# Optimization experiments

Hardware: AMD Instinct MI355X
Metric: run time of the kernel (lower is better)

The kernel has to match this reference:

```python
import jax, jax.numpy as jnp
import numpy as np

B, S, E, H, Dh = 4, 2048, 2048, 16, 128
EPS = 1e-6

def rms_norm(x, scale):
    # RMSNorm over last dim (the module calls it LayerNorm but uses mean of squares)
    x = x.astype(jnp.float32)
    mean2 = jnp.mean(jnp.square(x), axis=-1, keepdims=True)
    return (x * jax.lax.rsqrt(mean2 + EPS)) * scale

def setup_inputs() -> dict:
    key = jax.random.key(0)
    ks = jax.random.split(key, 8)
    sd = 1.0 / np.sqrt(E)
    Wq = jax.random.normal(ks[0], (E, H, Dh), jnp.float32) * sd / np.sqrt(Dh)  # query_init divides by sqrt(head_dim)
    Wk = jax.random.normal(ks[1], (E, H, Dh), jnp.float32) * sd
    Wv = jax.random.normal(ks[2], (E, H, Dh), jnp.float32) * sd
    Wo = jax.random.normal(ks[3], (H, Dh, E), jnp.float32) * (1.0 / np.sqrt(H * Dh))
    return {
        "inputs_q": jax.random.normal(ks[4], (B, S, E), jnp.float32),
        "inputs_kv": jax.random.normal(ks[5], (B, S, E), jnp.float32),
        "Wq": Wq, "Wk": Wk, "Wv": Wv,
        "q_ln_scale": jnp.ones((Dh,), jnp.float32),
        "k_ln_scale": jnp.ones((Dh,), jnp.float32),
        "Wo": Wo,
    }

def reference(inputs_q, inputs_kv, Wq, Wk, Wv, q_ln_scale, k_ln_scale, Wo):
    # QKV projections: [B,S,E] x [E,H,Dh] -> [B,S,H,Dh]
    q = jnp.einsum('bqe,ehd->bqhd', inputs_q, Wq)
    k = jnp.einsum('bke,ehd->bkhd', inputs_kv, Wk)
    v = jnp.einsum('bke,ehd->bkhd', inputs_kv, Wv)
    # QK RMS-norm before attention (the non-standard fusion-defeating step)
    q = rms_norm(q, q_ln_scale)
    k = rms_norm(k, k_ln_scale)
    # attention logits and softmax (no mask/bias, deterministic)
    logits = jnp.einsum('bqhd,bkhd->bhqk', q, k)
    probs = jax.nn.softmax(logits, axis=-1)
    # weighted values and output projection
    ctx = jnp.einsum('bhqk,bkhd->bqhd', probs, v)
    out = jnp.einsum('bqhd,hde->bqe', ctx, Wo)
    return out
```

## Files before the change

### kernel.cpp

```cpp
#include <hip/hip_runtime.h>
#include <hip/hip_bf16.h>

typedef unsigned short u16;
typedef unsigned int u32;
typedef _Float16 f16;
typedef __attribute__((ext_vector_type(8))) short bf16x8;
typedef __attribute__((ext_vector_type(8))) _Float16 f16x8;
typedef __attribute__((ext_vector_type(4))) float f32x4;
typedef __attribute__((ext_vector_type(4))) u16 u16x4;

__device__ __forceinline__ float bf2f(u16 u){ return __uint_as_float(((u32)u) << 16); }
__device__ __forceinline__ u16 f2bf(float f){
  u32 u = __float_as_uint(f);
  u += 0x7fffu + ((u >> 16) & 1u);
  return (u16)(u >> 16);
}
__device__ __forceinline__ void gll16(const u16* g, u16* l){
  __builtin_amdgcn_global_load_lds((const __attribute__((address_space(1))) u32*)g,
                                   (__attribute__((address_space(3))) u32*)l, 16, 0, 0);
}

#define MFMA16(a,b,c) __builtin_amdgcn_mfma_f32_16x16x32_bf16((a),(b),(c),0,0,0)
#define MFMAH(a,b,c)  __builtin_amdgcn_mfma_f32_16x16x32_f16((a),(b),(c),0,0,0)

__global__ __launch_bounds__(256) void cvt_f16_2(const float* __restrict__ in0, const float* __restrict__ in1,
                                                 u16* __restrict__ out0, u16* __restrict__ out1){
  const int half = blockIdx.x >> 13;
  const float* in = half ? in1 : in0;
  u16* out = half ? out1 : out0;
  const size_t i = ((size_t)(blockIdx.x & 8191)*256 + threadIdx.x)*8;
  f16 h[8];
  #pragma unroll
  for (int j=0;j<8;j++) h[j] = (f16)in[i+j];
  *(f16x8*)(out+i) = *(f16x8*)h;
}

__global__ __launch_bounds__(256) void transpose_w4(const float* __restrict__ w0, const float* __restrict__ w1,
                                                    const float* __restrict__ w2, const float* __restrict__ w3,
                                                    u16* __restrict__ o0, u16* __restrict__ o1,
                                                    u16* __restrict__ o2, u16* __restrict__ o3){
  const int z = blockIdx.z;
  const float* in = (z==0) ? w0 : (z==1) ? w1 : (z==2) ? w2 : w3;
  u16* oh = (z==0) ? o0 : (z==1) ? o1 : (z==2) ? o2 : o3;
  __shared__ float tile[64*68];
  const int t = threadIdx.x;
  const int r0 = blockIdx.y*64, c0 = blockIdx.x*64;
  #pragma unroll
  for (int p=0;p<2;p++){
    const int row = p*32 + (t>>3), cg = (t&7)*8;
    const float* s = in + (size_t)(r0+row)*2048 + c0 + cg;
    #pragma unroll
    for (int j=0;j<8;j++) tile[row*68 + cg + j] = s[j];
  }
  __syncthreads();
  #pragma unroll
  for (int p=0;p<2;p++){
    const int orow = p*32 + (t>>3), cg = (t&7)*8;
    f16 h[8];
    #pragma unroll
    for (int j=0;j<8;j++) h[j] = (f16)(tile[(cg+j)*68 + orow] * 256.f);
    *(f16x8*)(oh + (size_t)(c0+orow)*2048 + r0 + cg) = *(f16x8*)h;
  }
}

template<int EPI>
__global__ __launch_bounds__(512, 1) void gemm8(const u16* __restrict__ A,
                                                const u16* __restrict__ Bt,
                                                const float* __restrict__ scale,
                                                u16* __restrict__ C,
                                                float* __restrict__ Cf){
  constexpr int K = 2048, NT = 32;
  __shared__ __align__(16) u16 AL[2][2][8192];
  __shared__ __align__(16) u16 BL[2][2][8192];
  __shared__ float red[2][4][128];

  const int t = threadIdx.x;
  const int lane = t & 63, w = t >> 6;
  const int wm = w >> 2, wn = w & 3;
  const int l15 = lane & 15, l4 = lane >> 4;

  const int bid = blockIdx.x;
  const int xcd = bid & 7, q = bid >> 3;
  const int m0 = (((xcd >> 1) << 3) + (q >> 2)) * 256;
  const int n0 = (((xcd & 1) << 2) + (q & 3)) * 256;

  const int srow = t >> 2;
  const int skg = (t & 3) ^ ((srow ^ (srow >> 2)) & 3);
  const u16* gA = A  + (size_t)(m0 + srow) * K + skg * 8;
  const u16* gB = Bt + (size_t)(n0 + srow) * K + skg * 8;
  const int d0 = (w * 64) * 8;
  const int d1 = (512 + w * 64) * 8;

  const int sz = (l15 ^ (l15 >> 2)) & 3;
  const int kgp = ((l4 ^ sz) & 3) * 8;
  const int aoff = (wm * 128 + l15) * 32 + kgp;
  const int boff = (wn * 64 + l15) * 32 + kgp;

  f32x4 acc[8][4] = {};

#define STG_A(tile, kh, db) { const u16* s_ = gA + (size_t)(tile)*64 + (kh)*32; \
    gll16(s_, &AL[db][kh][0] + d0); gll16(s_ + (size_t)128*K, &AL[db][kh][0] + d1); }
#define STG_B(tile, kh, db) { const u16* s_ = gB + (size_t)(tile)*64 + (kh)*32; \
    gll16(s_, &BL[db][kh][0] + d0); gll16(s_ + (size_t)128*K, &BL[db][kh][0] + d1); }

  STG_A(0,0,0); STG_B(0,0,0);
  STG_A(0,1,0); STG_B(0,1,0);
  STG_A(1,0,1); STG_B(1,0,1);
  asm volatile("s_waitcnt vmcnt(4)" ::: "memory");
  __builtin_amdgcn_s_barrier();

  for (int g = 0; g < NT; ++g){
    const int db = g & 1, db1 = db ^ 1;
    const int t1 = (g+1 < NT) ? g+1 : NT-1;
    const int t2 = (g+2 < NT) ? g+2 : NT-1;
    f16x8 a[4], b[4];

    #pragma unroll
    for (int nf=0; nf<4; nf++) b[nf] = *(const f16x8*)&BL[db][0][boff + nf*512];
    #pragma unroll
    for (int mf=0; mf<4; mf++) a[mf] = *(const f16x8*)&AL[db][0][aoff + mf*512];
    STG_A(t1, 1, db1);
    __builtin_amdgcn_s_barrier();
    asm volatile("s_waitcnt lgkmcnt(0)" ::: "memory");
    __builtin_amdgcn_sched_barrier(0);
    __builtin_amdgcn_s_setprio(1);
    #pragma unroll
    for (int mf=0; mf<4; mf++)
      #pragma unroll
      for (int nf=0; nf<4; nf++)
        acc[mf][nf] = MFMAH(a[mf], b[nf], acc[mf][nf]);
    __builtin_amdgcn_s_setprio(0);
    __builtin_amdgcn_s_barrier();

    #pragma unroll
    for (int mf=0; mf<4; mf++) a[mf] = *(const f16x8*)&AL[db][0][aoff + (mf+4)*512];
    STG_B(t1, 1, db1);
    __builtin_amdgcn_s_barrier();
    asm volatile("s_waitcnt lgkmcnt(0)" ::: "memory");
    __builtin_amdgcn_sched_barrier(0);
    __builtin_amdgcn_s_setprio(1);
    #pragma unroll
    for (int mf=0; mf<4; mf++)
      #pragma unroll
      for (int nf=0; nf<4; nf++)
        acc[mf+4][nf] = MFMAH(a[mf], b[nf], acc[mf+4][nf]);
    __builtin_amdgcn_s_setprio(0);
    __builtin_amdgcn_s_barrier();

    #pragma unroll
    for (int nf=0; nf<4; nf++) b[nf] = *(const f16x8*)&BL[db][1][boff + nf*512];
    #pragma unroll
    for (int mf=0; mf<4; mf++) a[mf] = *(const f16x8*)&AL[db][1][aoff + mf*512];
    STG_A(t2, 0, db);
    __builtin_amdgcn_s_barrier();
    asm volatile("s_waitcnt lgkmcnt(0)" ::: "memory");
    __builtin_amdgcn_sched_barrier(0);
    __builtin_amdgcn_s_setprio(1);
    #pragma unroll
    for (int mf=0; mf<4; mf++)
      #pragma unroll
      for (int nf=0; nf<4; nf++)
        acc[mf][nf] = MFMAH(a[mf], b[nf], acc[mf][nf]);
    __builtin_amdgcn_s_setprio(0);
    __builtin_amdgcn_s_barrier();

    #pragma unroll
    for (int mf=0; mf<4; mf++) a[mf] = *(const f16x8*)&AL[db][1][aoff + (mf+4)*512];
    STG_B(t2, 0, db);
    __builtin_amdgcn_s_barrier();
    asm volatile("s_waitcnt lgkmcnt(0)" ::: "memory");
    __builtin_amdgcn_sched_barrier(0);
    __builtin_amdgcn_s_setprio(1);
    #pragma unroll
    for (int mf=0; mf<4; mf++)
      #pragma unroll
      for (int nf=0; nf<4; nf++)
        acc[mf+4][nf] = MFMAH(a[mf], b[nf], acc[mf+4][nf]);
    __builtin_amdgcn_s_setprio(0);
    asm volatile("s_waitcnt vmcnt(4)" ::: "memory");
    __builtin_amdgcn_s_barrier();
  }

  asm volatile("s_waitcnt vmcnt(0)" ::: "memory");
  __builtin_amdgcn_s_barrier();

  const float us = 1.f/256.f;
  if (EPI == 0){
    #pragma unroll
    for (int mf=0; mf<8; mf++)
      #pragma unroll
      for (int nf=0; nf<4; nf++)
        #pragma unroll
        for (int r=0;r<4;r++) acc[mf][nf][r] *= us;
    #pragma unroll
    for (int mf=0; mf<8; mf++){
      #pragma unroll
      for (int r=0;r<4;r++){
        float p = acc[mf][0][r]*acc[mf][0][r] + acc[mf][1][r]*acc[mf][1][r]
                + acc[mf][2][r]*acc[mf][2][r] + acc[mf][3][r]*acc[mf][3][r];
        #pragma unroll
        for (int d=1; d<16; d<<=1) p += __shfl_xor(p, d, 64);
        if (l15 == 0) red[wm][wn][mf*16 + l4*4 + r] = p;
      }
    }
    __syncthreads();
    float sc[4];
    #pragma unroll
    for (int nf=0; nf<4; nf++) sc[nf] = scale[(wn*64 + nf*16 + l15) & 127];
    #pragma unroll
    for (int mf=0; mf<8; mf++){
      #pragma unroll
      for (int r=0;r<4;r++){
        const int rl = mf*16 + l4*4 + r;
        const float inv = rsqrtf((red[wm][wn & 2][rl] + red[wm][(wn & 2) | 1][rl])*(1.f/128.f) + 1e-6f);
        const size_t grow = (size_t)(m0 + wm*128 + rl);
        #pragma unroll
        for (int nf=0; nf<4; nf++){
          f16 hv = (f16)(acc[mf][nf][r]*inv*sc[nf]);
          C[grow*2048 + (n0 + wn*64 + nf*16 + l15)] = *reinterpret_cast<u16*>(&hv);
        }
      }
    }
  } else if (EPI == 1){
    #pragma unroll
    for (int mf=0; mf<8; mf++){
      const int m = m0 + wm*128 + mf*16 + l4*4;
      const int bb = m >> 11, s = m & 2047;
      #pragma unroll
      for (int nf=0; nf<4; nf++){
        const int n = n0 + wn*64 + nf*16 + l15;
        u16x4 pk;
        pk.x = f2bf(acc[mf][nf][0]*us); pk.y = f2bf(acc[mf][nf][1]*us);
        pk.z = f2bf(acc[mf][nf][2]*us); pk.w = f2bf(acc[mf][nf][3]*us);
        *(u16x4*)&C[((size_t)(bb*16 + (n>>7))*128 + (n&127))*2048 + s] = pk;
      }
    }
  } else {
    #pragma unroll
    for (int mf=0; mf<8; mf++){
      const size_t r0 = (size_t)(m0 + wm*128 + mf*16 + l4*4);
      #pragma unroll
      for (int nf=0; nf<4; nf++){
        const int c = n0 + wn*64 + nf*16 + l15;
        #pragma unroll
        for (int r=0;r<4;r++)
          Cf[(r0+r)*2048 + c] = acc[mf][nf][r]*us;
      }
    }
  }
#undef STG_A
#undef STG_B
}

__global__ __launch_bounds__(256, 2) void attn_fwd(const u16* __restrict__ Qh_,
                                                   const u16* __restrict__ Kh_,
                                                   const u16* __restrict__ Vt, u16* __restrict__ O){
  __shared__ __align__(16) u16 Ksh[2][64*128];
  __shared__ __align__(16) u16 Vsh[128*64];
  __shared__ __align__(16) u16 Psh[4][32*72];
  const int t = threadIdx.x;
  const int lane = t & 63, w = t >> 6;
  const int l15 = lane & 15, l4 = lane >> 4;
  const int lin = blockIdx.x;
  const int bh  = (lin & 7)*8 + (lin >> 7);
  const int qt  = (lin >> 3) & 15;
  const int b = bh >> 4, h = bh & 15;
  const int q0 = qt*128 + w*32;

  f16x8 qh[2][4];
  #pragma unroll
  for (int qf=0;qf<2;qf++){
    const size_t qoff = ((size_t)((b<<11) + q0 + qf*16 + l15)*16 + h)*128 + l4*8;
    #pragma unroll
    for (int kk=0;kk<4;kk++)
      qh[qf][kk] = *(const f16x8*)(Qh_ + qoff + kk*32);
  }
  f32x4 oacc[2][8] = {};
  float lpart[2][4] = {};

  size_t ksrc[4], vsrc[4];
  #pragma unroll
  for (int p=0;p<4;p++){
    const int g = p*256 + t;
    ksrc[p] = ((size_t)((b<<11) + (g>>4))*16 + h)*128 + (size_t)((((g&15) ^ ((g>>4)&7))*8));
    vsrc[p] = ((size_t)(b*16 + h)*128 + (g>>3))*2048 + (size_t)((((g&7) ^ ((g>>3)&7))*8));
  }

#define STK(T, DB) { const size_t ko_ = (size_t)(T)*131072; \
    _Pragma("unroll") for (int p_=0;p_<4;p_++) gll16(Kh_ + ksrc[p_] + ko_, &Ksh[DB][0] + (p_*256+t)*8); }
#define STV(T) { const int vo_ = (T)*64; \
    _Pragma("unroll") for (int p_=0;p_<4;p_++) gll16(Vt + vsrc[p_] + vo_, &Vsh[0] + (p_*256+t)*8); }

  STK(0,0); STV(0); STK(1,1);
  asm volatile("s_waitcnt vmcnt(4)" ::: "memory");
  __builtin_amdgcn_s_barrier();

  for (int tt = 0; tt < 32; ++tt){
    const int c = tt & 1;

    f32x4 sa[2][4] = {};
    #pragma unroll
    for (int ks=0;ks<4;ks++){
      const int row = ks*16 + l15;
      #pragma unroll
      for (int kk=0;kk<4;kk++){
        const int off = row*128 + (((kk*4 + l4) ^ (row&7))*8);
        f16x8 khf = *(const f16x8*)&Ksh[c][off];
        sa[0][ks] = MFMAH(qh[0][kk], khf, sa[0][ks]);
        sa[1][ks] = MFMAH(qh[1][kk], khf, sa[1][ks]);
      }
    }
    #pragma unroll
    for (int qf=0;qf<2;qf++)
      #pragma unroll
      for (int r=0;r<4;r++){
        float rs = 0.f;
        #pragma unroll
        for (int ks=0;ks<4;ks++){
          const float e = __expf(sa[qf][ks][r] - 24.f);
          rs += e;
          Psh[w][(qf*16 + l4*4 + r)*72 + ks*16 + l15] = f2bf(e);
        }
        lpart[qf][r] += rs;
      }
    asm volatile("s_waitcnt vmcnt(4) lgkmcnt(0)" ::: "memory");
    __builtin_amdgcn_sched_barrier(0);
    __builtin_amdgcn_s_barrier();

    #pragma unroll
    for (int ks2=0;ks2<2;ks2++){
      bf16x8 pa0 = *(const bf16x8*)&Psh[w][(l15)*72 + ks2*32 + l4*8];
      bf16x8 pa1 = *(const bf16x8*)&Psh[w][(16 + l15)*72 + ks2*32 + l4*8];
      #pragma unroll
      for (int n=0;n<8;n++){
        const int row = n*16 + l15;
        const int c8 = ks2*4 + l4;
        bf16x8 vb = *(const bf16x8*)&Vsh[row*64 + ((c8 ^ (row&7))*8)];
        oacc[0][n] = MFMA16(pa0, vb, oacc[0][n]);
        oacc[1][n] = MFMA16(pa1, vb, oacc[1][n]);
      }
    }
    __builtin_amdgcn_s_barrier();

    const int tv = (tt+1 < 32) ? tt+1 : 31;
    const int tk = (tt+2 < 32) ? tt+2 : 31;
    STV(tv); STK(tk, c);
    asm volatile("s_waitcnt vmcnt(8)" ::: "memory");
    __builtin_amdgcn_s_barrier();
  }
  asm volatile("s_waitcnt vmcnt(0)" ::: "memory");

#undef STK
#undef STV

  #pragma unroll
  for (int qf=0;qf<2;qf++){
    float lrun[4];
    #pragma unroll
    for (int r=0;r<4;r++){
      float s = lpart[qf][r];
      #pragma unroll
      for (int d=1; d<16; d<<=1) s += __shfl_xor(s, d, 64);
      lrun[r] = s;
    }
    #pragma unroll
    for (int n=0;n<8;n++){
      const int d = n*16 + l15;
      #pragma unroll
      for (int r=0;r<4;r++){
        const int s = q0 + qf*16 + l4*4 + r;
        f16 hv = (f16)(oacc[qf][n][r] / lrun[r]);
        O[((size_t)((b<<11) + s)*16 + h)*128 + d] = *reinterpret_cast<u16*>(&hv);
      }
    }
  }
}

extern "C" void kernel_launch(void* const* d_in, const int* in_sizes, int n_in,
                              void* d_out, int out_size, void* d_ws, size_t ws_size,
                              hipStream_t stream){
  const float* f_inq = (const float*)d_in[0];
  const float* f_inkv= (const float*)d_in[1];
  const float* f_Wq  = (const float*)d_in[2];
  const float* f_Wk  = (const float*)d_in[3];
  const float* f_Wv  = (const float*)d_in[4];
  const float* scq   = (const float*)d_in[5];
  const float* sck   = (const float*)d_in[6];
  const float* f_Wo  = (const float*)d_in[7];

  u16* ws = (u16*)d_ws;
  const size_t ACT = (size_t)16777216;
  const size_t WEL = (size_t)4194304;
  u16* q_h = ws;
  u16* k_h = q_h + ACT;
  u16* v_t = k_h + ACT;
  u16* ctx = v_t + ACT;
  u16* wq  = ctx + ACT;
  u16* wk  = wq + WEL;
  u16* wv  = wk + WEL;
  u16* wo  = wv + WEL;

  u16* inq16  = (u16*)d_out;
  u16* inkv16 = inq16 + ACT;

  cvt_f16_2<<<16384, 256, 0, stream>>>(f_inq, f_inkv, inq16, inkv16);

  transpose_w4<<<dim3(32,32,4), 256, 0, stream>>>(f_Wq, f_Wk, f_Wv, f_Wo, wq, wk, wv, wo);

  gemm8<0><<<256, 512, 0, stream>>>(inq16,  wq, scq, q_h, nullptr);
  gemm8<0><<<256, 512, 0, stream>>>(inkv16, wk, sck, k_h, nullptr);
  gemm8<1><<<256, 512, 0, stream>>>(inkv16, wv, nullptr, v_t, nullptr);

  attn_fwd<<<dim3(1024), 256, 0, stream>>>(q_h, k_h, v_t, ctx);

  gemm8<2><<<256, 512, 0, stream>>>(ctx, wo, nullptr, nullptr, (float*)d_out);
}
```

Measured before the change: 523.2 us.

## Load V fragments directly from global into registers and merge prep kernels

```diff
diff --git a/kernel.cpp b/kernel.cpp
--- a/kernel.cpp
+++ b/kernel.cpp
@@ -23,28 +23,31 @@
 #define MFMA16(a,b,c) __builtin_amdgcn_mfma_f32_16x16x32_bf16((a),(b),(c),0,0,0)
 #define MFMAH(a,b,c)  __builtin_amdgcn_mfma_f32_16x16x32_f16((a),(b),(c),0,0,0)
 
-__global__ __launch_bounds__(256) void cvt_f16_2(const float* __restrict__ in0, const float* __restrict__ in1,
-                                                 u16* __restrict__ out0, u16* __restrict__ out1){
-  const int half = blockIdx.x >> 13;
-  const float* in = half ? in1 : in0;
-  u16* out = half ? out1 : out0;
-  const size_t i = ((size_t)(blockIdx.x & 8191)*256 + threadIdx.x)*8;
-  f16 h[8];
-  #pragma unroll
-  for (int j=0;j<8;j++) h[j] = (f16)in[i+j];
-  *(f16x8*)(out+i) = *(f16x8*)h;
-}
-
-__global__ __launch_bounds__(256) void transpose_w4(const float* __restrict__ w0, const float* __restrict__ w1,
-                                                    const float* __restrict__ w2, const float* __restrict__ w3,
-                                                    u16* __restrict__ o0, u16* __restrict__ o1,
-                                                    u16* __restrict__ o2, u16* __restrict__ o3){
-  const int z = blockIdx.z;
+__global__ __launch_bounds__(256) void prep(const float* __restrict__ inq, const float* __restrict__ inkv,
+                                            u16* __restrict__ oq, u16* __restrict__ okv,
+                                            const float* __restrict__ w0, const float* __restrict__ w1,
+                                            const float* __restrict__ w2, const float* __restrict__ w3,
+                                            u16* __restrict__ o0, u16* __restrict__ o1,
+                                            u16* __restrict__ o2, u16* __restrict__ o3){
+  __shared__ float tile[64*68];
+  const int bid = blockIdx.x;
+  const int t = threadIdx.x;
+  if (bid < 16384){
+    const int half = bid >> 13;
+    const float* in = half ? inkv : inq;
+    u16* out = half ? okv : oq;
+    const size_t i = ((size_t)(bid & 8191)*256 + t)*8;
+    f16 h[8];
+    #pragma unroll
+    for (int j=0;j<8;j++) h[j] = (f16)in[i+j];
+    *(f16x8*)(out+i) = *(f16x8*)h;
+    return;
+  }
+  const int r = bid - 16384;
+  const int z = r >> 10, b2 = r & 1023;
   const float* in = (z==0) ? w0 : (z==1) ? w1 : (z==2) ? w2 : w3;
   u16* oh = (z==0) ? o0 : (z==1) ? o1 : (z==2) ? o2 : o3;
-  __shared__ float tile[64*68];
-  const int t = threadIdx.x;
-  const int r0 = blockIdx.y*64, c0 = blockIdx.x*64;
+  const int r0 = (b2 >> 5)*64, c0 = (b2 & 31)*64;
   #pragma unroll
   for (int p=0;p<2;p++){
     const int row = p*32 + (t>>3), cg = (t&7)*8;
@@ -256,7 +259,6 @@
                                                    const u16* __restrict__ Kh_,
                                                    const u16* __restrict__ Vt, u16* __restrict__ O){
   __shared__ __align__(16) u16 Ksh[2][64*128];
-  __shared__ __align__(16) u16 Vsh[128*64];
   __shared__ __align__(16) u16 Psh[4][32*72];
   const int t = threadIdx.x;
   const int lane = t & 63, w = t >> 6;
@@ -278,20 +280,18 @@
   f32x4 oacc[2][8] = {};
   float lpart[2][4] = {};
 
-  size_t ksrc[4], vsrc[4];
+  size_t ksrc[4];
   #pragma unroll
   for (int p=0;p<4;p++){
     const int g = p*256 + t;
     ksrc[p] = ((size_t)((b<<11) + (g>>4))*16 + h)*128 + (size_t)((((g&15) ^ ((g>>4)&7))*8));
-    vsrc[p] = ((size_t)(b*16 + h)*128 + (g>>3))*2048 + (size_t)((((g&7) ^ ((g>>3)&7))*8));
-  }
+  }
+  const u16* vg = Vt + (size_t)(b*16 + h)*262144 + (size_t)l15*2048 + l4*8;
 
 #define STK(T, DB) { const size_t ko_ = (size_t)(T)*131072; \
     _Pragma("unroll") for (int p_=0;p_<4;p_++) gll16(Kh_ + ksrc[p_] + ko_, &Ksh[DB][0] + (p_*256+t)*8); }
-#define STV(T) { const int vo_ = (T)*64; \
-    _Pragma("unroll") for (int p_=0;p_<4;p_++) gll16(Vt + vsrc[p_] + vo_, &Vsh[0] + (p_*256+t)*8); }
-
-  STK(0,0); STV(0); STK(1,1);
+
+  STK(0,0); STK(1,1);
   asm volatile("s_waitcnt vmcnt(4)" ::: "memory");
   __builtin_amdgcn_s_barrier();
 
@@ -310,6 +310,10 @@
         sa[1][ks] = MFMAH(qh[1][kk], khf, sa[1][ks]);
       }
     }
+    bf16x8 vb0[8];
+    #pragma unroll
+    for (int n=0;n<8;n++) vb0[n] = *(const bf16x8*)(vg + (size_t)n*32768 + tt*64);
+
     #pragma unroll
     for (int qf=0;qf<2;qf++)
       #pragma unroll
@@ -323,35 +327,38 @@
         }
         lpart[qf][r] += rs;
       }
-    asm volatile("s_waitcnt vmcnt(4) lgkmcnt(0)" ::: "memory");
+    asm volatile("s_waitcnt lgkmcnt(0)" ::: "memory");
     __builtin_amdgcn_sched_barrier(0);
     __builtin_amdgcn_s_barrier();
 
-    #pragma unroll
-    for (int ks2=0;ks2<2;ks2++){
-      bf16x8 pa0 = *(const bf16x8*)&Psh[w][(l15)*72 + ks2*32 + l4*8];
-      bf16x8 pa1 = *(const bf16x8*)&Psh[w][(16 + l15)*72 + ks2*32 + l4*8];
+    bf16x8 vb1[8];
+    #pragma unroll
+    for (int n=0;n<8;n++) vb1[n] = *(const bf16x8*)(vg + (size_t)n*32768 + tt*64 + 32);
+    const int tk = (tt+2 < 32) ? tt+2 : 31;
+    STK(tk, c);
+
+    {
+      bf16x8 pa0 = *(const bf16x8*)&Psh[w][l15*72 + l4*8];
+      bf16x8 pa1 = *(const bf16x8*)&Psh[w][(16 + l15)*72 + l4*8];
       #pragma unroll
       for (int n=0;n<8;n++){
-        const int row = n*16 + l15;
-        const int c8 = ks2*4 + l4;
-        bf16x8 vb = *(const bf16x8*)&Vsh[row*64 + ((c8 ^ (row&7))*8)];
-        oacc[0][n] = MFMA16(pa0, vb, oacc[0][n]);
-        oacc[1][n] = MFMA16(pa1, vb, oacc[1][n]);
-      }
-    }
-    __builtin_amdgcn_s_barrier();
-
-    const int tv = (tt+1 < 32) ? tt+1 : 31;
-    const int tk = (tt+2 < 32) ? tt+2 : 31;
-    STV(tv); STK(tk, c);
-    asm volatile("s_waitcnt vmcnt(8)" ::: "memory");
+        oacc[0][n] = MFMA16(pa0, vb0[n], oacc[0][n]);
+        oacc[1][n] = MFMA16(pa1, vb0[n], oacc[1][n]);
+      }
+      bf16x8 pb0 = *(const bf16x8*)&Psh[w][l15*72 + 32 + l4*8];
+      bf16x8 pb1 = *(const bf16x8*)&Psh[w][(16 + l15)*72 + 32 + l4*8];
+      #pragma unroll
+      for (int n=0;n<8;n++){
+        oacc[0][n] = MFMA16(pb0, vb1[n], oacc[0][n]);
+        oacc[1][n] = MFMA16(pb1, vb1[n], oacc[1][n]);
+      }
+    }
+    asm volatile("s_waitcnt vmcnt(4)" ::: "memory");
     __builtin_amdgcn_s_barrier();
   }
   asm volatile("s_waitcnt vmcnt(0)" ::: "memory");
 
 #undef STK
-#undef STV
 
   #pragma unroll
   for (int qf=0;qf<2;qf++){
@@ -403,9 +410,8 @@
   u16* inq16  = (u16*)d_out;
   u16* inkv16 = inq16 + ACT;
 
-  cvt_f16_2<<<16384, 256, 0, stream>>>(f_inq, f_inkv, inq16, inkv16);
-
-  transpose_w4<<<dim3(32,32,4), 256, 0, stream>>>(f_Wq, f_Wk, f_Wv, f_Wo, wq, wk, wv, wo);
+  prep<<<20480, 256, 0, stream>>>(f_inq, f_inkv, inq16, inkv16,
+                                  f_Wq, f_Wk, f_Wv, f_Wo, wq, wk, wv, wo);
 
   gemm8<0><<<256, 512, 0, stream>>>(inq16,  wq, scq, q_h, nullptr);
   gemm8<0><<<256, 512, 0, stream>>>(inkv16, wk, sck, k_h, nullptr);
```

Result: slower. 617.8 us (+18.1%).
